# Optimization experiments

Measured on AMD Instinct MI355X. Metric: run time of the kernel, lower is better.

The kernel has to match this reference:

```python
import jax, jax.numpy as jnp
import numpy as np

D_MODEL = 1024
N_HEADS = 16
D_HEAD = D_MODEL // N_HEADS


def setup_inputs() -> dict:
    key = jax.random.key(0)
    k1, k2, k3 = jax.random.split(key, 3)
    B, T = 2, 2048
    x = jax.random.normal(k1, (B, T, D_MODEL), dtype=jnp.float32)
    # Linear weights stored as (in, out), equivalent to torch W^T
    w_qkv = jax.random.normal(k2, (D_MODEL, 3 * D_MODEL), dtype=jnp.float32) * (D_MODEL ** -0.5)
    w_proj = jax.random.normal(k3, (D_MODEL, D_MODEL), dtype=jnp.float32) * (D_MODEL ** -0.5)
    return {"x": x, "w_qkv": w_qkv, "w_proj": w_proj}


def reference(x, w_qkv, w_proj):
    B, T, C = x.shape
    qkv = x @ w_qkv                                   # (B, T, 3C)
    qkv = qkv.reshape(B, T, 3, N_HEADS, D_HEAD)
    q, k, v = qkv[:, :, 0], qkv[:, :, 1], qkv[:, :, 2]  # (B, T, H, dh)
    q = q.transpose(0, 2, 1, 3)                        # (B, H, T, dh)
    k = k.transpose(0, 2, 1, 3)
    v = v.transpose(0, 2, 1, 3)
    scale = 1.0 / jnp.sqrt(jnp.float32(D_HEAD))
    scores = jnp.einsum('bhqd,bhkd->bhqk', q, k) * scale  # (B, H, T, T)
    causal = jnp.tril(jnp.ones((T, T), dtype=bool))
    scores = jnp.where(causal, scores, jnp.float32(-jnp.inf))
    w = jax.nn.softmax(scores, axis=-1)
    ctx = jnp.einsum('bhqk,bhkd->bhqd', w, v)          # (B, H, T, dh)
    ctx = ctx.transpose(0, 2, 1, 3).reshape(B, T, C)
    return ctx @ w_proj
```

## Files before the change

kernel.cpp:

```cpp
#include <hip/hip_runtime.h>
#include <hip/hip_bf16.h>
#include <math.h>
#include <stdint.h>

#define D_MODEL 1024
#define NHEADS  16
#define DHEAD   64
#define BATCH   2
#define SEQ     2048
#define ROWS    (BATCH*SEQ)

#define NEG_BIG (-1e30f)
#define QSCALE  0.18033688011112042f

typedef __bf16 bf16v8 __attribute__((ext_vector_type(8)));
typedef short  shortv8 __attribute__((ext_vector_type(8)));
typedef short  shortv4 __attribute__((ext_vector_type(4)));
typedef float  floatv4 __attribute__((ext_vector_type(4)));
typedef unsigned short ush;

__device__ __forceinline__ ush f2b(float f) {
  return __builtin_bit_cast(ush, (__bf16)f);
}

__device__ __forceinline__ void async16(ush* lds, const ush* g) {
  __builtin_amdgcn_global_load_lds(
      (const __attribute__((address_space(1))) void*)g,
      (__attribute__((address_space(3))) void*)lds, 16, 0, 0);
}

__global__ __launch_bounds__(256)
void prep(const uint32_t* __restrict__ x, ush* __restrict__ xb,
          const void* __restrict__ wqkv, ush* __restrict__ wqkvT,
          const void* __restrict__ wproj, ush* __restrict__ wprojT,
          int* __restrict__ flagp) {
  __shared__ int sflag;
  __shared__ __align__(16) ush tile[64][72];

  int bid = blockIdx.x;
  int t   = threadIdx.x;

  if (t < 64) {
    uint32_t e = (x[t] >> 7) & 0xFF;
    unsigned long long m = __ballot(e >= 96 && e <= 144);
    if (t == 0) sflag = (__popcll(m) >= 32) ? 1 : 0;
  }
  __syncthreads();
  int isbf = sflag;
  if (bid == 0 && t == 0) *flagp = isbf;

  if (bid < 2048) {
    size_t i = (size_t)bid * 256 + t;
    if (isbf) {
      ((shortv8*)xb)[i] = ((const shortv8*)x)[i];
    } else {
      const floatv4* p = ((const floatv4*)x) + i * 2;
      floatv4 a = p[0], b = p[1];
      shortv8 o;
#pragma unroll
      for (int j = 0; j < 4; ++j) { o[j] = (short)f2b(a[j]); o[4+j] = (short)f2b(b[j]); }
      ((shortv8*)xb)[i] = o;
    }
  } else {
    const void* W; ush* Wt; int N, b2;
    const int K = 1024;
    if (bid < 2816) { W = wqkv;  Wt = wqkvT;  N = 3072; b2 = bid - 2048; }
    else            { W = wproj; Wt = wprojT; N = 1024; b2 = bid - 2816; }
    int tiles_n = N >> 6;
    int tk = b2 / tiles_n;
    int tn = b2 % tiles_n;
    int r  = t >> 2;
    int c8 = (t & 3) * 8;

    if (isbf) {
      const ush* src = (const ush*)W + (size_t)(tk*64 + r) * N + tn*64;
#pragma unroll
      for (int c = 0; c < 2; ++c)
        *(shortv8*)&tile[r][c8 + c*32] = *(const shortv8*)&src[c8 + c*32];
    } else {
      const float* src = (const float*)W + (size_t)(tk*64 + r) * N + tn*64;
#pragma unroll
      for (int c = 0; c < 2; ++c) {
        const floatv4* p = (const floatv4*)&src[c8 + c*32];
        floatv4 a = p[0], b = p[1];
        shortv8 o;
#pragma unroll
        for (int j = 0; j < 4; ++j) { o[j] = (short)f2b(a[j]); o[4+j] = (short)f2b(b[j]); }
        *(shortv8*)&tile[r][c8 + c*32] = o;
      }
    }
    __syncthreads();
    ush* dst = Wt + (size_t)(tn*64 + r) * K + tk*64;
#pragma unroll
    for (int c = 0; c < 2; ++c) {
      int k8 = c8 + c*32;
      shortv8 v;
#pragma unroll
      for (int j = 0; j < 8; ++j) v[j] = (short)tile[k8 + j][r];
      *(shortv8*)&dst[k8] = v;
    }
  }
}

#define MFMA16(a,b,c) __builtin_amdgcn_mfma_f32_16x16x32_bf16(a,b,c,0,0,0)

__global__ __launch_bounds__(512, 2)
void gemm_qkv(const ush* __restrict__ A, const ush* __restrict__ Bt,
              ush* __restrict__ qb_, ush* __restrict__ kb_, ush* __restrict__ vb_) {
  __shared__ __align__(16) ush smem[65536];
  const int K = 1024;
  const int tiles_n = 12;
  int bid = blockIdx.x;
  int m0 = (bid / tiles_n) * 256;
  int n0 = (bid % tiles_n) * 256;
  int t    = threadIdx.x;
  int lane = t & 63;
  int w    = t >> 6;
  int wr   = w >> 2;
  int wc   = w & 3;
  int lr   = lane & 15;
  int quad = lane >> 4;
  int r8   = lane >> 3;
  int s8   = lane & 7;
  int g8   = s8 ^ r8;

  int aeo = 2*w + (w>>2)*8;
  int alo = aeo + 8;
  int beo = (w>>1)*8 + (w&1)*2;
  int blo = beo + 4;

  const ush* gAe0 = A  + (size_t)(m0 + aeo*8     + r8)*K + g8*8;
  const ush* gAe1 = gAe0 + (size_t)8*K;
  const ush* gAl0 = A  + (size_t)(m0 + alo*8     + r8)*K + g8*8;
  const ush* gAl1 = gAl0 + (size_t)8*K;
  const ush* gBe0 = Bt + (size_t)(n0 + beo*8     + r8)*K + g8*8;
  const ush* gBe1 = gBe0 + (size_t)8*K;
  const ush* gBl0 = Bt + (size_t)(n0 + blo*8     + r8)*K + g8*8;
  const ush* gBl1 = gBl0 + (size_t)8*K;

  int lAe0 = aeo*512,         lAe1 = lAe0 + 512;
  int lAl0 = alo*512,         lAl1 = lAl0 + 512;
  int lBe0 = 32768 + beo*512, lBe1 = lBe0 + 512;
  int lBl0 = 32768 + blo*512, lBl1 = lBl0 + 512;

  floatv4 acc[4][8] = {};
  bf16v8 af[4][2];
  bf16v8 bf[4][2];

  int sk0 = ((quad    ) ^ (lr & 7)) * 8;
  int sk1 = ((quad + 4) ^ (lr & 7)) * 8;

  async16(&smem[lAe0], gAe0); async16(&smem[lAe1], gAe1);
  async16(&smem[lBe0], gBe0); async16(&smem[lBe1], gBe1);
  async16(&smem[lBl0], gBl0); async16(&smem[lBl1], gBl1);
  async16(&smem[lAl0], gAl0); async16(&smem[lAl1], gAl1);

  for (int kt = 0; kt < 16; ++kt) {
    int cur = kt & 1, nx = cur ^ 1;
    int kn  = (kt + 1 < 16) ? (kt + 1) : 15;
    int ko  = kn * 64;
    int nb  = nx * 16384;

    const ush* Ab = &smem[cur*16384 + (wr*128 + lr)*64];
    const ush* Bb = &smem[32768 + cur*16384 + (wc*64 + lr)*64];

    asm volatile("s_waitcnt vmcnt(4)" ::: "memory");
    __builtin_amdgcn_s_barrier();

#pragma unroll
    for (int mi = 0; mi < 4; ++mi) {
      af[mi][0] = *(const bf16v8*)&Ab[mi*1024 + sk0];
      af[mi][1] = *(const bf16v8*)&Ab[mi*1024 + sk1];
    }
#pragma unroll
    for (int ni = 0; ni < 2; ++ni) {
      bf[ni][0] = *(const bf16v8*)&Bb[ni*1024 + sk0];
      bf[ni][1] = *(const bf16v8*)&Bb[ni*1024 + sk1];
    }
    async16(&smem[nb + lAe0], gAe0 + ko); async16(&smem[nb + lAe1], gAe1 + ko);
    __builtin_amdgcn_s_setprio(1);
#pragma unroll
    for (int ni = 0; ni < 2; ++ni)
#pragma unroll
      for (int mi = 0; mi < 4; ++mi)
#pragma unroll
        for (int ks = 0; ks < 2; ++ks)
          acc[ni][mi] = MFMA16(bf[ni][ks], af[mi][ks], acc[ni][mi]);
    __builtin_amdgcn_s_setprio(0);

    asm volatile("s_waitcnt vmcnt(4)" ::: "memory");
    __builtin_amdgcn_s_barrier();

#pragma unroll
    for (int ni = 0; ni < 2; ++ni) {
      bf[2+ni][0] = *(const bf16v8*)&Bb[(2+ni)*1024 + sk0];
      bf[2+ni][1] = *(const bf16v8*)&Bb[(2+ni)*1024 + sk1];
    }
    async16(&smem[nb + lBe0], gBe0 + ko); async16(&smem[nb + lBe1], gBe1 + ko);
    __builtin_amdgcn_s_setprio(1);
#pragma unroll
    for (int ni = 0; ni < 2; ++ni)
#pragma unroll
      for (int mi = 0; mi < 4; ++mi)
#pragma unroll
        for (int ks = 0; ks < 2; ++ks)
          acc[2+ni][mi] = MFMA16(bf[2+ni][ks], af[mi][ks], acc[2+ni][mi]);
    __builtin_amdgcn_s_setprio(0);

    asm volatile("s_waitcnt vmcnt(4)" ::: "memory");
    __builtin_amdgcn_s_barrier();

#pragma unroll
    for (int mi = 0; mi < 4; ++mi) {
      af[mi][0] = *(const bf16v8*)&Ab[4096 + mi*1024 + sk0];
      af[mi][1] = *(const bf16v8*)&Ab[4096 + mi*1024 + sk1];
    }
    async16(&smem[nb + lBl0], gBl0 + ko); async16(&smem[nb + lBl1], gBl1 + ko);
    __builtin_amdgcn_s_setprio(1);
#pragma unroll
    for (int ni = 0; ni < 2; ++ni)
#pragma unroll
      for (int mi = 0; mi < 4; ++mi)
#pragma unroll
        for (int ks = 0; ks < 2; ++ks)
          acc[ni][4+mi] = MFMA16(bf[ni][ks], af[mi][ks], acc[ni][4+mi]);
    __builtin_amdgcn_s_setprio(0);

    __builtin_amdgcn_s_barrier();

    async16(&smem[nb + lAl0], gAl0 + ko); async16(&smem[nb + lAl1], gAl1 + ko);
    __builtin_amdgcn_s_setprio(1);
#pragma unroll
    for (int ni = 0; ni < 2; ++ni)
#pragma unroll
      for (int mi = 0; mi < 4; ++mi)
#pragma unroll
        for (int ks = 0; ks < 2; ++ks)
          acc[2+ni][4+mi] = MFMA16(bf[2+ni][ks], af[mi][ks], acc[2+ni][4+mi]);
    __builtin_amdgcn_s_setprio(0);
  }

  asm volatile("s_waitcnt vmcnt(0)" ::: "memory");
  __builtin_amdgcn_s_barrier();

  int s   = n0 >> 10;
  int h   = ((n0 & 1023) + wc*64) >> 6;
  int b   = (m0 + wr*128) >> 11;
  int bh  = b*16 + h;
  int ttw = (m0 + wr*128) & 2047;

  if (s < 2) {
    ush* dst = (s == 0) ? qb_ : kb_;
    float sc = (s == 0) ? QSCALE : 1.0f;
#pragma unroll
    for (int ni = 0; ni < 4; ++ni) {
      int d4 = ni*16 + quad*4;
#pragma unroll
      for (int mi = 0; mi < 8; ++mi) {
        int tt = ttw + mi*16 + lr;
        shortv4 v4;
#pragma unroll
        for (int r = 0; r < 4; ++r) v4[r] = (short)f2b(acc[ni][mi][r] * sc);
        *(shortv4*)&dst[((size_t)bh*SEQ + tt)*64 + d4] = v4;
      }
    }
  } else {
    ush* L = &smem[w*4096];
#pragma unroll
    for (int th = 0; th < 2; ++th) {
      int tw = ttw + th*64;
#pragma unroll
      for (int ni = 0; ni < 4; ++ni) {
#pragma unroll
        for (int r = 0; r < 4; ++r) {
          int dl = ni*16 + quad*4 + r;
          shortv4 p4;
#pragma unroll
          for (int j = 0; j < 4; ++j) p4[j] = (short)f2b(acc[ni][th*4 + j][r]);
          int slot = (lr >> 1) ^ (dl & 7);
          *(shortv4*)&L[dl*64 + slot*8 + (lr & 1)*4] = p4;
        }
      }
#pragma unroll
      for (int p = 0; p < 8; ++p) {
        int dl = p*8 + (lane >> 3);
        int c8 = lane & 7;
        int slot = c8 ^ (dl & 7);
        shortv8 v = *(shortv8*)&L[dl*64 + slot*8];
        *(shortv8*)&vb_[((size_t)bh*64 + dl)*SEQ + tw + c8*8] = v;
      }
    }
  }
}

__global__ __launch_bounds__(256, 4)
void gemm_bt(const ush* __restrict__ A, const ush* __restrict__ Bt,
             void* __restrict__ Cp, const int* __restrict__ flag,
             int ldc, int tiles_n) {
  __shared__ __align__(16) ush smem[12288];
  const int K = 1024;
  int bid = blockIdx.x;
  int m0 = (bid / tiles_n) * 64;
  int n0 = (bid % tiles_n) * 128;
  int t    = threadIdx.x;
  int lane = t & 63;
  int w    = t >> 6;
  int wm   = (w >> 1) * 32;
  int wn   = (w & 1) * 64;
  int lr   = lane & 15;
  int quad = lane >> 4;
  floatv4 acc[4][2] = {};
  int r16 = lane >> 2;
  int g4  = (lane & 3) ^ (r16 & 3);
  const ush* gA0 = A  + (size_t)(m0 + 16*w + r16)*K + g4*8;
  const ush* gB0 = Bt + (size_t)(n0 + 32*w + r16)*K + g4*8;
  const ush* gB1 = gB0 + (size_t)16*K;
  int fs = (quad ^ (lr & 3)) * 8;

  async16(&smem[(16*w)*32], gA0);
  async16(&smem[4096 + (32*w)*32], gB0);
  async16(&smem[4096 + (32*w+16)*32], gB1);

  for (int kk = 0; kk < K; kk += 32) {
    int cur = (kk >> 5) & 1;
    __syncthreads();
    if (kk + 32 < K) {
      int nx = cur ^ 1;
      async16(&smem[nx*2048 + (16*w)*32], gA0 + kk + 32);
      async16(&smem[4096 + nx*4096 + (32*w)*32], gB0 + kk + 32);
      async16(&smem[4096 + nx*4096 + (32*w+16)*32], gB1 + kk + 32);
    }
    bf16v8 af[2], bfr[4];
#pragma unroll
    for (int j = 0; j < 2; ++j)
      af[j] = *(bf16v8*)&smem[cur*2048 + (wm + j*16 + lr)*32 + fs];
#pragma unroll
    for (int i = 0; i < 4; ++i)
      bfr[i] = *(bf16v8*)&smem[4096 + cur*4096 + (wn + i*16 + lr)*32 + fs];
#pragma unroll
    for (int i = 0; i < 4; ++i)
#pragma unroll
      for (int j = 0; j < 2; ++j)
        acc[i][j] = __builtin_amdgcn_mfma_f32_16x16x32_bf16(bfr[i], af[j],
                                                            acc[i][j], 0, 0, 0);
  }

  int f32out = (flag != nullptr) && (*flag == 0);
  if (f32out) {
    float* Cf = (float*)Cp;
#pragma unroll
    for (int i = 0; i < 4; ++i) {
      int nb = n0 + wn + i*16 + quad*4;
#pragma unroll
      for (int j = 0; j < 2; ++j) {
        int row = m0 + wm + j*16 + lr;
        *(floatv4*)&Cf[(size_t)row*ldc + nb] = acc[i][j];
      }
    }
  } else {
    __hip_bfloat16* Cb = (__hip_bfloat16*)Cp;
#pragma unroll
    for (int i = 0; i < 4; ++i) {
      int nb = n0 + wn + i*16 + quad*4;
#pragma unroll
      for (int j = 0; j < 2; ++j) {
        int row = m0 + wm + j*16 + lr;
        shortv4 v4;
#pragma unroll
        for (int r = 0; r < 4; ++r) v4[r] = (short)f2b(acc[i][j][r]);
        *(shortv4*)&((ush*)Cb)[(size_t)row*ldc + nb] = v4;
      }
    }
  }
}

#define PSTR 72

__device__ __forceinline__ void softpack(const floatv4* s, int qw, int kb0,
                                         bool diag, ush* PsW, int quad, int lr) {
  if (diag) {
#pragma unroll
    for (int r = 0; r < 4; ++r) {
      int qv = qw + quad*4 + r;
      shortv4 p4;
#pragma unroll
      for (int j = 0; j < 4; ++j) {
        float z = (kb0 + 16*j + lr > qv) ? NEG_BIG : s[j][r];
        p4[j] = (short)f2b(__builtin_amdgcn_exp2f(z));
      }
      *(shortv4*)&PsW[(quad*4 + r)*PSTR + lr*4] = p4;
    }
  } else {
#pragma unroll
    for (int r = 0; r < 4; ++r) {
      shortv4 p4;
#pragma unroll
      for (int j = 0; j < 4; ++j)
        p4[j] = (short)f2b(__builtin_amdgcn_exp2f(s[j][r]));
      *(shortv4*)&PsW[(quad*4 + r)*PSTR + lr*4] = p4;
    }
  }
}

__global__ __launch_bounds__(512, 4)
void attn_fwd(const ush* __restrict__ qb_, const ush* __restrict__ kb_,
              const ush* __restrict__ vb_, __hip_bfloat16* __restrict__ ctx) {
  __shared__ __align__(16) ush Ks[2][64*64];
  __shared__ __align__(16) ush Vt[2][64*64];
  __shared__ __align__(16) ush Ps[8][16*PSTR];

  int bid = blockIdx.x;
  int p   = bid & 15;
  int h   = (bid >> 4) & 15;
  int b   = bid >> 8;
  int bh  = b*16 + h;

  int t = threadIdx.x, w8 = t >> 6, lane = t & 63, lr = lane & 15, quad = lane >> 4;
  int isB = w8 >> 2;
  int w   = w8 & 3;

  const ush* qh = qb_ + (size_t)bh * SEQ * 64;
  const ush* kh = kb_ + (size_t)bh * SEQ * 64;
  const ush* vh = vb_ + (size_t)bh * 64 * SEQ;

  int qt = isB ? (31 - p) : p;
  int qw = qt*64 + w*16;

  const ush* qp = qh + (size_t)(qw + lr)*64;
  bf16v8 qf0 = *(const bf16v8*)&qp[quad*8];
  bf16v8 qf1 = *(const bf16v8*)&qp[32 + quad*8];

  floatv4 acc[4] = {}, acl = {};

  bf16v8 ones;
#pragma unroll
  for (int j = 0; j < 8; ++j) ones[j] = (__bf16)1.0f;

  int r8 = lane >> 3;
  int s8 = lane & 7;
  int g8 = s8 ^ r8;
  const ush* kg = kh + (size_t)(8*w8 + r8)*64 + g8*8;
  const ush* vg = vh + (size_t)(8*w8 + r8)*SEQ + g8*8;
  int lo = (8*w8)*64;

  int sl0 = quad ^ (lr & 7);
  int sl1 = (quad + 4) ^ (lr & 7);

  int ntiles = 32 - p;

  async16(&Ks[0][lo], kg);
  async16(&Vt[0][lo], vg);

  for (int tk = 0; tk < ntiles; ++tk) {
    int cur = tk & 1;
    __syncthreads();
    if (tk + 1 < ntiles) {
      int nx = cur ^ 1;
      async16(&Ks[nx][lo], kg + (size_t)(tk + 1) * 64 * 64);
      async16(&Vt[nx][lo], vg + (size_t)(tk + 1) * 64);
    }

    bool live = isB | (tk <= p);
    if (live) {
      int kb0 = tk * 64;
      bool diag = (tk == qt);

      floatv4 s[4] = {};
      __builtin_amdgcn_s_setprio(1);
#pragma unroll
      for (int j = 0; j < 4; ++j) {
        if (!diag || j <= w) {
          int row = 16*j + lr;
          bf16v8 kf0 = *(bf16v8*)&Ks[cur][row*64 + sl0*8];
          bf16v8 kf1 = *(bf16v8*)&Ks[cur][row*64 + sl1*8];
          s[j] = MFMA16(qf0, kf0, s[j]);
          s[j] = MFMA16(qf1, kf1, s[j]);
        }
      }
      __builtin_amdgcn_s_setprio(0);

      softpack(s, qw, kb0, diag, &Ps[w8][0], quad, lr);

      bf16v8 pf0 = *(bf16v8*)&Ps[w8][lr*PSTR + quad*8];
      bf16v8 pf1 = *(bf16v8*)&Ps[w8][lr*PSTR + 32 + quad*8];

      __builtin_amdgcn_s_setprio(1);
      acl = MFMA16(pf0, ones, acl);
      acl = MFMA16(pf1, ones, acl);

#pragma unroll
      for (int c = 0; c < 4; ++c) {
        int row = 16*c + lr;
        bf16v8 vf0 = *(bf16v8*)&Vt[cur][row*64 + sl0*8];
        bf16v8 vf1 = *(bf16v8*)&Vt[cur][row*64 + sl1*8];
        acc[c] = MFMA16(pf0, vf0, acc[c]);
        acc[c] = MFMA16(pf1, vf1, acc[c]);
      }
      __builtin_amdgcn_s_setprio(0);
    }
  }

#pragma unroll
  for (int r = 0; r < 4; ++r) {
    float inv = 1.0f / fmaxf(acl[r], 1e-30f);
    size_t o = (size_t)(b*SEQ + qw + quad*4 + r) * D_MODEL + h*64;
#pragma unroll
    for (int c = 0; c < 4; ++c)
      ctx[o + c*16 + lr] = __float2bfloat16(acc[c][r] * inv);
  }
}

extern "C" void kernel_launch(void* const* d_in, const int* in_sizes, int n_in,
                              void* d_out, int out_size, void* d_ws, size_t ws_size,
                              hipStream_t stream) {
  const void* x      = d_in[0];
  const void* w_qkv  = d_in[1];
  const void* w_proj = d_in[2];

  int* flag   = (int*)d_ws;
  ush* xb     = (ush*)d_ws + 8;
  ush* wqkvT  = xb     + (size_t)ROWS * D_MODEL;
  ush* wprojT = wqkvT  + (size_t)3072 * 1024;
  ush* qbuf   = wprojT + (size_t)1024 * 1024;
  ush* kbuf   = qbuf   + (size_t)32 * SEQ * 64;
  ush* vbuf   = kbuf   + (size_t)32 * SEQ * 64;
  ush* ctx    = xb;

  prep<<<3072, 256, 0, stream>>>((const uint32_t*)x, xb,
                                 w_qkv, wqkvT, w_proj, wprojT, flag);

  gemm_qkv<<<192, 512, 0, stream>>>(xb, wqkvT, qbuf, kbuf, vbuf);

  attn_fwd<<<BATCH * NHEADS * 16, 512, 0, stream>>>(
      qbuf, kbuf, vbuf, (__hip_bfloat16*)ctx);

  gemm_bt<<<(ROWS/64)*(1024/128), 256, 0, stream>>>(
      ctx, wprojT, d_out, flag, 1024, 1024/128);
}
```

Baseline: 178.5 us.

## Split attention blocks to one query tile each with explicit vmcnt pipelining

Before, each 512-thread block paired two query tiles (p and 31-p) that shared K/V loads. Now each 256-thread block handles a single query tile, and blocks are launched heaviest-first. The double-buffer sync is rewritten from __syncthreads to raw s_barrier with an explicit s_waitcnt vmcnt(4), so the next tile's async loads stay in flight during compute. This removes the idle waves on dead tiles of the paired scheme but loses K/V reuse across the pair and adds a redundant prefetch on the last iteration.

```diff
diff --git a/kernel.cpp b/kernel.cpp
--- a/kernel.cpp
+++ b/kernel.cpp
@@ -402,28 +402,25 @@
   }
 }
 
-__global__ __launch_bounds__(512, 4)
+__global__ __launch_bounds__(256, 3)
 void attn_fwd(const ush* __restrict__ qb_, const ush* __restrict__ kb_,
               const ush* __restrict__ vb_, __hip_bfloat16* __restrict__ ctx) {
   __shared__ __align__(16) ush Ks[2][64*64];
   __shared__ __align__(16) ush Vt[2][64*64];
-  __shared__ __align__(16) ush Ps[8][16*PSTR];
+  __shared__ __align__(16) ush Ps[4][16*PSTR];
 
   int bid = blockIdx.x;
-  int p   = bid & 15;
-  int h   = (bid >> 4) & 15;
-  int b   = bid >> 8;
-  int bh  = b*16 + h;
-
-  int t = threadIdx.x, w8 = t >> 6, lane = t & 63, lr = lane & 15, quad = lane >> 4;
-  int isB = w8 >> 2;
-  int w   = w8 & 3;
+  int qt  = 31 - (bid & 31);
+  int bh  = bid >> 5;
+  int h   = bh & 15;
+  int b   = bh >> 4;
+
+  int t = threadIdx.x, w = t >> 6, lane = t & 63, lr = lane & 15, quad = lane >> 4;
 
   const ush* qh = qb_ + (size_t)bh * SEQ * 64;
   const ush* kh = kb_ + (size_t)bh * SEQ * 64;
   const ush* vh = vb_ + (size_t)bh * 64 * SEQ;
 
-  int qt = isB ? (31 - p) : p;
   int qw = qt*64 + w*16;
 
   const ush* qp = qh + (size_t)(qw + lr)*64;
@@ -439,66 +436,71 @@
   int r8 = lane >> 3;
   int s8 = lane & 7;
   int g8 = s8 ^ r8;
-  const ush* kg = kh + (size_t)(8*w8 + r8)*64 + g8*8;
-  const ush* vg = vh + (size_t)(8*w8 + r8)*SEQ + g8*8;
-  int lo = (8*w8)*64;
+  const ush* kg0 = kh + (size_t)(16*w     + r8)*64 + g8*8;
+  const ush* kg1 = kh + (size_t)(16*w + 8 + r8)*64 + g8*8;
+  const ush* vg0 = vh + (size_t)(16*w     + r8)*SEQ + g8*8;
+  const ush* vg1 = vh + (size_t)(16*w + 8 + r8)*SEQ + g8*8;
+  int lo0 = (16*w)*64, lo1 = (16*w + 8)*64;
 
   int sl0 = quad ^ (lr & 7);
   int sl1 = (quad + 4) ^ (lr & 7);
 
-  int ntiles = 32 - p;
-
-  async16(&Ks[0][lo], kg);
-  async16(&Vt[0][lo], vg);
+  int ntiles = qt + 1;
+
+  async16(&Ks[0][lo0], kg0); async16(&Ks[0][lo1], kg1);
+  async16(&Vt[0][lo0], vg0); async16(&Vt[0][lo1], vg1);
 
   for (int tk = 0; tk < ntiles; ++tk) {
-    int cur = tk & 1;
-    __syncthreads();
-    if (tk + 1 < ntiles) {
-      int nx = cur ^ 1;
-      async16(&Ks[nx][lo], kg + (size_t)(tk + 1) * 64 * 64);
-      async16(&Vt[nx][lo], vg + (size_t)(tk + 1) * 64);
-    }
-
-    bool live = isB | (tk <= p);
-    if (live) {
-      int kb0 = tk * 64;
-      bool diag = (tk == qt);
-
-      floatv4 s[4] = {};
-      __builtin_amdgcn_s_setprio(1);
-#pragma unroll
-      for (int j = 0; j < 4; ++j) {
-        if (!diag || j <= w) {
-          int row = 16*j + lr;
-          bf16v8 kf0 = *(bf16v8*)&Ks[cur][row*64 + sl0*8];
-          bf16v8 kf1 = *(bf16v8*)&Ks[cur][row*64 + sl1*8];
-          s[j] = MFMA16(qf0, kf0, s[j]);
-          s[j] = MFMA16(qf1, kf1, s[j]);
-        }
-      }
-      __builtin_amdgcn_s_setprio(0);
-
-      softpack(s, qw, kb0, diag, &Ps[w8][0], quad, lr);
-
-      bf16v8 pf0 = *(bf16v8*)&Ps[w8][lr*PSTR + quad*8];
-      bf16v8 pf1 = *(bf16v8*)&Ps[w8][lr*PSTR + 32 + quad*8];
-
-      __builtin_amdgcn_s_setprio(1);
-      acl = MFMA16(pf0, ones, acl);
-      acl = MFMA16(pf1, ones, acl);
-
-#pragma unroll
-      for (int c = 0; c < 4; ++c) {
-        int row = 16*c + lr;
-        bf16v8 vf0 = *(bf16v8*)&Vt[cur][row*64 + sl0*8];
-        bf16v8 vf1 = *(bf16v8*)&Vt[cur][row*64 + sl1*8];
-        acc[c] = MFMA16(pf0, vf0, acc[c]);
-        acc[c] = MFMA16(pf1, vf1, acc[c]);
-      }
-      __builtin_amdgcn_s_setprio(0);
-    }
-  }
+    int cur = tk & 1, nx = cur ^ 1;
+
+    __builtin_amdgcn_s_barrier();
+    {
+      int tn = (tk + 1 < ntiles) ? (tk + 1) : tk;
+      size_t ko = (size_t)tn * 4096, vo = (size_t)tn * 64;
+      async16(&Ks[nx][lo0], kg0 + ko); async16(&Ks[nx][lo1], kg1 + ko);
+      async16(&Vt[nx][lo0], vg0 + vo); async16(&Vt[nx][lo1], vg1 + vo);
+    }
+    asm volatile("s_waitcnt vmcnt(4)" ::: "memory");
+    __builtin_amdgcn_s_barrier();
+
+    int kb0 = tk * 64;
+    bool diag = (tk == qt);
+
+    floatv4 s[4] = {};
+    __builtin_amdgcn_s_setprio(1);
+#pragma unroll
+    for (int j = 0; j < 4; ++j) {
+      if (!diag || j <= w) {
+        int row = 16*j + lr;
+        bf16v8 kf0 = *(bf16v8*)&Ks[cur][row*64 + sl0*8];
+        bf16v8 kf1 = *(bf16v8*)&Ks[cur][row*64 + sl1*8];
+        s[j] = MFMA16(qf0, kf0, s[j]);
+        s[j] = MFMA16(qf1, kf1, s[j]);
+      }
+    }
+    __builtin_amdgcn_s_setprio(0);
+
+    softpack(s, qw, kb0, diag, &Ps[w][0], quad, lr);
+
+    bf16v8 pf0 = *(bf16v8*)&Ps[w][lr*PSTR + quad*8];
+    bf16v8 pf1 = *(bf16v8*)&Ps[w][lr*PSTR + 32 + quad*8];
+
+    __builtin_amdgcn_s_setprio(1);
+    acl = MFMA16(pf0, ones, acl);
+    acl = MFMA16(pf1, ones, acl);
+
+#pragma unroll
+    for (int c = 0; c < 4; ++c) {
+      int row = 16*c + lr;
+      bf16v8 vf0 = *(bf16v8*)&Vt[cur][row*64 + sl0*8];
+      bf16v8 vf1 = *(bf16v8*)&Vt[cur][row*64 + sl1*8];
+      acc[c] = MFMA16(pf0, vf0, acc[c]);
+      acc[c] = MFMA16(pf1, vf1, acc[c]);
+    }
+    __builtin_amdgcn_s_setprio(0);
+  }
+
+  asm volatile("s_waitcnt vmcnt(0)" ::: "memory");
 
 #pragma unroll
   for (int r = 0; r < 4; ++r) {
@@ -531,7 +533,7 @@
 
   gemm_qkv<<<192, 512, 0, stream>>>(xb, wqkvT, qbuf, kbuf, vbuf);
 
-  attn_fwd<<<BATCH * NHEADS * 16, 512, 0, stream>>>(
+  attn_fwd<<<BATCH * NHEADS * 32, 256, 0, stream>>>(
       qbuf, kbuf, vbuf, (__hip_bfloat16*)ctx);
 
   gemm_bt<<<(ROWS/64)*(1024/128), 256, 0, stream>>>(
```

After: 209.2 us. +17.2%, slower.
